# Kernel tuning notes

Hardware: AMD Instinct MI355X
Metric: run time of the kernel (lower is better)

The kernel has to match this reference:

```python
import jax, jax.numpy as jnp
import numpy as np

EPS = 1e-5  # float32 path of the torch LayerNorm variants


def setup_inputs() -> dict:
    key = jax.random.key(0)
    ks = jax.random.split(key, 12)
    b, c, t, h, w = 2, 512, 16, 32, 32
    heads, dim_head = 8, 64
    inner = heads * dim_head            # 512
    cpb = c // 2                        # 256 (ContinuousPositionBias hidden dim)
    inner_ff = int(c * 4 * 2 / 3)       # 1365 (GEGLU FeedForward)
    s = 0.02
    return {
        "x": jax.random.normal(ks[0], (b, c, t, h, w), jnp.float32),
        "framerate": 4,
        "g_norm": jnp.ones((c,), jnp.float32),
        "Wq": jax.random.normal(ks[1], (c, inner), jnp.float32) * s,
        "Wkv": jax.random.normal(ks[2], (c, 2 * inner), jnp.float32) * s,
        "Wo": jax.random.normal(ks[3], (inner, c), jnp.float32) * s,
        "pos_emb": jax.random.normal(ks[4], (1, 30, c), jnp.float32),
        "fr_emb": jax.random.normal(ks[5], (1, 30, c), jnp.float32),
        "cpb_w1": jax.random.normal(ks[6], (1, cpb), jnp.float32) * s,
        "cpb_b1": jnp.zeros((cpb,), jnp.float32),
        "cpb_w2": jax.random.normal(ks[7], (cpb, cpb), jnp.float32) * s,
        "cpb_b2": jnp.zeros((cpb,), jnp.float32),
        "cpb_w3": jax.random.normal(ks[8], (cpb, 8), jnp.float32) * s,
        "cpb_b3": jnp.zeros((8,), jnp.float32),
        "Win": jax.random.normal(ks[9], (c, 2 * inner_ff), jnp.float32) * s,
        "chan_g": jnp.ones((inner_ff,), jnp.float32),
        "Wout": jax.random.normal(ks[10], (inner_ff, c), jnp.float32) * s,
    }


def _forward(x, framerate, g_norm, Wq, Wkv, Wo, pos_emb, fr_emb,
             cpb_w1, cpb_b1, cpb_w2, cpb_b2, cpb_w3, cpb_b3,
             Win, chan_g, Wout):
    b, c, t, hh, ww = x.shape
    heads = cpb_b3.shape[0]
    dim_head = Wq.shape[1] // heads
    scale = dim_head ** -0.5

    # ---- ContinuousPositionBias over time (num_dims=1, log_dist) ----
    pos = jnp.arange(t)
    rel = (pos[:, None] - pos[None, :])[..., None].astype(x.dtype)   # [t, t, 1]
    rel = jnp.sign(rel) * jnp.log(jnp.abs(rel) + 1.0)
    hb = jax.nn.silu(rel @ cpb_w1 + cpb_b1)
    hb = jax.nn.silu(hb @ cpb_w2 + cpb_b2)
    bias = jnp.transpose(hb @ cpb_w3 + cpb_b3, (2, 0, 1))            # [H, t, t]

    # ---- temporal attention: fold spatial dims into batch ----
    xt = jnp.transpose(x, (0, 3, 4, 2, 1)).reshape(b * hh * ww, t, c)  # [B, t, c]
    xe = xt + pos_emb[:, :t] + fr_emb[:, framerate - 1:framerate]
    # LayerNorm as written in the source: stats over dim=1 (the token axis)
    mean = jnp.mean(xe, axis=1, keepdims=True)
    var = jnp.var(xe, axis=1, keepdims=True)
    xn = (xe - mean) * jax.lax.rsqrt(jnp.maximum(var, EPS)) * g_norm

    q = (xn @ Wq).reshape(-1, t, heads, dim_head).transpose(0, 2, 1, 3)  # [B,H,t,d]
    k, v = jnp.split(xn @ Wkv, 2, axis=-1)
    k = k.reshape(-1, t, heads, dim_head).transpose(0, 2, 1, 3)
    v = v.reshape(-1, t, heads, dim_head).transpose(0, 2, 1, 3)

    sim = jnp.einsum('bhid,bhjd->bhij', q * scale, k) + bias[None]
    attn = jax.nn.softmax(sim, axis=-1)
    o = jnp.einsum('bhij,bhjd->bhid', attn, v)
    o = o.transpose(0, 2, 1, 3).reshape(-1, t, heads * dim_head) @ Wo
    xt = o + xt  # residual
    x = jnp.transpose(xt.reshape(b, hh, ww, t, c), (0, 4, 3, 1, 2))  # [b,c,t,h,w]

    # ---- GEGLU FeedForward (1x1x1 convs) with token shift over time ----
    y = jnp.einsum('bcthw,co->bothw', x, Win)
    y1, gate = jnp.split(y, 2, axis=1)
    y = y1 * jax.nn.gelu(gate, approximate=False)
    half = (y.shape[1] + 1) // 2  # torch.chunk: first chunk gets ceil
    ya, yb = y[:, :half], y[:, half:]
    yb = jnp.pad(yb, ((0, 0), (0, 0), (1, 0), (0, 0), (0, 0)))[:, :, :-1]
    y = jnp.concatenate([ya, yb], axis=1)
    m = jnp.mean(y, axis=1, keepdims=True)
    vv = jnp.var(y, axis=1, keepdims=True)
    y = (y - m) * jax.lax.rsqrt(jnp.maximum(vv, EPS)) * chan_g[None, :, None, None, None]
    y = jnp.einsum('bcthw,co->bothw', y, Wout)
    return y + x


def reference(x, framerate, g_norm, Wq, Wkv, Wo, pos_emb, fr_emb,
              cpb_w1, cpb_b1, cpb_w2, cpb_b2, cpb_w3, cpb_b3,
              Win, chan_g, Wout):
    return _forward(x, framerate, g_norm, Wq, Wkv, Wo, pos_emb, fr_emb,
                    cpb_w1, cpb_b1, cpb_w2, cpb_b2, cpb_w3, cpb_b3,
                    Win, chan_g, Wout)
```

## Files before the change

kernel.cpp:

```cpp
#include <hip/hip_runtime.h>

using u16 = unsigned short;
using f32x4 = __attribute__((ext_vector_type(4))) float;
using short8 = __attribute__((ext_vector_type(8))) short;

__device__ __forceinline__ float bf2f(u16 u) {
    union { unsigned int i; float f; } v; v.i = ((unsigned int)u) << 16; return v.f;
}
__device__ __forceinline__ u16 f2bf(float f) {
    union { float f; unsigned int i; } v; v.f = f;
    unsigned int u = v.i;
    u += 0x7fffu + ((u >> 16) & 1u);
    return (u16)(u >> 16);
}
__device__ __forceinline__ void gload16(const u16* g, u16* l) {
    __builtin_amdgcn_global_load_lds((const __attribute__((address_space(1))) void*)g,
                                     (__attribute__((address_space(3))) void*)l, 16, 0, 0);
}

__global__ __launch_bounds__(256) void prep_weights(
    const float* __restrict__ Wq, const float* __restrict__ Wkv,
    const float* __restrict__ Wo, const float* __restrict__ Win,
    const float* __restrict__ Wout, const float* __restrict__ cg,
    u16* __restrict__ wqkvt, u16* __restrict__ wot,
    u16* __restrict__ winp, u16* __restrict__ woutt)
{
    int i = blockIdx.x * 256 + threadIdx.x;
    if (i < 1536 * 512) {
        int n = i >> 9, c = i & 511;
        float v = (n < 512) ? Wq[c * 512 + n] : Wkv[c * 1024 + (n - 512)];
        wqkvt[i] = f2bf(v); return;
    }
    i -= 1536 * 512;
    if (i < 512 * 512) {
        int cc = i >> 9, k = i & 511;
        wot[i] = f2bf(Wo[k * 512 + cc]); return;
    }
    i -= 512 * 512;
    if (i < 2816 * 512) {
        int n = i >> 9, c = i & 511;
        int jj = ((n >> 5) << 4) + (n & 15);
        int gate = (n >> 4) & 1;
        float v = (jj < 1365) ? Win[c * 2730 + jj + gate * 1365] : 0.f;
        winp[i] = f2bf(v); return;
    }
    i -= 2816 * 512;
    if (i < 512 * 1408) {
        int cc = i / 1408, j = i % 1408;
        float v = (j < 1365) ? Wout[j * 512 + cc] * cg[j] : 0.f;
        woutt[i] = f2bf(v); return;
    }
}

__global__ __launch_bounds__(256) void ssum_kernel(
    const float* __restrict__ Wout, const float* __restrict__ cg, float* __restrict__ ssum)
{
    int c = blockIdx.x * 256 + threadIdx.x;
    if (c >= 512) return;
    float s = 0.f;
    for (int j = 0; j < 1365; ++j) s += Wout[j * 512 + c] * cg[j];
    ssum[c] = s;
}

__global__ __launch_bounds__(256) void bias_kernel(
    const float* __restrict__ w1, const float* __restrict__ b1,
    const float* __restrict__ w2, const float* __restrict__ b2,
    const float* __restrict__ w3, const float* __restrict__ b3,
    float* __restrict__ bias)
{
    __shared__ float h1[256], h2[256];
    int rc = blockIdx.x;
    int ti = rc >> 4, tj = rc & 15;
    int j = threadIdx.x;
    float r = (float)(ti - tj);
    float rl = (r > 0.f) ? logf(r + 1.f) : ((r < 0.f) ? -logf(1.f - r) : 0.f);
    float a = rl * w1[j] + b1[j];
    h1[j] = a / (1.f + __expf(-a));
    __syncthreads();
    float acc = b2[j];
    for (int k = 0; k < 256; ++k) acc += h1[k] * w2[k * 256 + j];
    h2[j] = acc / (1.f + __expf(-acc));
    __syncthreads();
    if (j < 8) {
        float ab = b3[j];
        for (int k = 0; k < 256; ++k) ab += h2[k] * w3[k * 8 + j];
        bias[j * 256 + ti * 16 + tj] = ab;
    }
}

__global__ __launch_bounds__(256) void k1_norm(
    const float* __restrict__ x, const int* __restrict__ frp,
    const float* __restrict__ g_norm, const float* __restrict__ pos_emb,
    const float* __restrict__ fr_emb,
    u16* __restrict__ xn, u16* __restrict__ xt)
{
    __shared__ u16 tile[256 * 34];
    const int bid = blockIdx.x;
    const int b = bid >> 10, rem = bid & 1023;
    const int hw0 = (rem >> 4) << 4;
    const int c0 = (rem & 15) << 5;
    const int tid = threadIdx.x;
    const int hwl = tid & 15, cl = tid >> 4;
    const int fr = frp[0] - 1;
    float v[2][16], mean2[2], ri2[2], gg2[2], fv2[2];
    for (int cp = 0; cp < 2; ++cp) {
        const int c = c0 + cl + (cp << 4);
        const float* xp = x + (size_t)(b * 512 + c) * 16384 + hw0 + hwl;
        const float fv = fr_emb[fr * 512 + c];
        float s1 = 0.f, s2 = 0.f;
#pragma unroll
        for (int t = 0; t < 16; ++t) {
            float xv = xp[t * 1024];
            v[cp][t] = xv;
            float xe = xv + pos_emb[t * 512 + c] + fv;
            s1 += xe; s2 += xe * xe;
        }
        float m = s1 * 0.0625f;
        float var = s2 * 0.0625f - m * m;
        mean2[cp] = m; ri2[cp] = rsqrtf(fmaxf(var, 1e-5f));
        gg2[cp] = g_norm[c]; fv2[cp] = fv;
    }
    for (int cp = 0; cp < 2; ++cp) {
        const int c = c0 + cl + (cp << 4);
#pragma unroll
        for (int t = 0; t < 16; ++t) {
            float xe = v[cp][t] + pos_emb[t * 512 + c] + fv2[cp];
            tile[((t << 4) + hwl) * 34 + cl + (cp << 4)] = f2bf((xe - mean2[cp]) * ri2[cp] * gg2[cp]);
        }
    }
    __syncthreads();
    for (int it = 0; it < 32; ++it) {
        int rowl = (tid >> 5) + (it << 3);
        int col = tid & 31;
        size_t p = (size_t)b * 16384 + (size_t)(rowl >> 4) * 1024 + hw0 + (rowl & 15);
        xn[p * 512 + c0 + col] = tile[rowl * 34 + col];
    }
    __syncthreads();
    for (int cp = 0; cp < 2; ++cp)
#pragma unroll
        for (int t = 0; t < 16; ++t)
            tile[((t << 4) + hwl) * 34 + cl + (cp << 4)] = f2bf(v[cp][t]);
    __syncthreads();
    for (int it = 0; it < 32; ++it) {
        int rowl = (tid >> 5) + (it << 3);
        int col = tid & 31;
        size_t p = (size_t)b * 16384 + (size_t)(rowl >> 4) * 1024 + hw0 + (rowl & 15);
        xt[p * 512 + c0 + col] = tile[rowl * 34 + col];
    }
}

template<int EPI>
__global__ __launch_bounds__(256, 2) void gemm_bt(
    const u16* __restrict__ A, const u16* __restrict__ B, int K, int Nb,
    u16* __restrict__ outb, float* __restrict__ outf,
    const u16* __restrict__ addb,
    const float* __restrict__ marr, const float* __restrict__ rinv,
    const float* __restrict__ ssum, int ldOut)
{
    __shared__ u16 lds[2 * 128 * 64];
    u16* lA = lds;
    u16* lB = lds + 128 * 64;
    const int tid = threadIdx.x, lane = tid & 63, w = tid >> 6;
    const int wr = w >> 1, wc = w & 1;
    const int cpx = gridDim.x >> 3;
    const int wgid = (blockIdx.x & 7) * cpx + (blockIdx.x >> 3);
    const int p0 = (wgid / Nb) * 128, n0 = (wgid % Nb) * 128;
    f32x4 acc[4][4] = {};
    for (int kt = 0; kt < K; kt += 64) {
        for (int i = 0; i < 4; ++i) {
            int rb = w * 4 + i;
            int r = rb * 8 + (lane >> 3);
            int cg = (lane & 7) ^ (r & 7);
            gload16(A + (size_t)(p0 + r) * K + (kt + cg * 8), lA + rb * 512);
            gload16(B + (size_t)(n0 + r) * K + (kt + cg * 8), lB + rb * 512);
        }
        __syncthreads();
#pragma unroll
        for (int kk = 0; kk < 2; ++kk) {
            short8 av[4], bv[4];
#pragma unroll
            for (int m = 0; m < 4; ++m) {
                int r = wr * 64 + m * 16 + (lane & 15);
                int cc = ((kk << 2) + (lane >> 4)) ^ (r & 7);
                av[m] = *(const short8*)(lA + r * 64 + cc * 8);
            }
#pragma unroll
            for (int n = 0; n < 4; ++n) {
                int r = wc * 64 + n * 16 + (lane & 15);
                int cc = ((kk << 2) + (lane >> 4)) ^ (r & 7);
                bv[n] = *(const short8*)(lB + r * 64 + cc * 8);
            }
#pragma unroll
            for (int m = 0; m < 4; ++m)
#pragma unroll
                for (int n = 0; n < 4; ++n)
                    acc[m][n] = __builtin_amdgcn_mfma_f32_16x16x32_bf16(av[m], bv[n], acc[m][n], 0, 0, 0);
        }
        __syncthreads();
    }

    if constexpr (EPI == 0 || EPI == 1) {
#pragma unroll
        for (int m = 0; m < 4; ++m)
#pragma unroll
            for (int n = 0; n < 4; ++n) {
                int row = p0 + wr * 64 + m * 16 + ((lane >> 4) << 2);
                int col = n0 + wc * 64 + n * 16 + (lane & 15);
#pragma unroll
                for (int r = 0; r < 4; ++r) {
                    float vv = acc[m][n][r];
                    if constexpr (EPI == 1) vv += bf2f(addb[(size_t)(row + r) * ldOut + col]);
                    outb[(size_t)(row + r) * ldOut + col] = f2bf(vv);
                }
            }
    } else if constexpr (EPI == 2) {
#pragma unroll
        for (int m = 0; m < 4; ++m)
#pragma unroll
            for (int np = 0; np < 2; ++np) {
                int nv = np << 1;
                int colBase = n0 + wc * 64 + nv * 16 + (lane & 15);
                int jj = ((colBase >> 5) << 4) + (colBase & 15);
                int rowb = p0 + wr * 64 + m * 16 + ((lane >> 4) << 2);
                int t = (rowb >> 10) & 15;
#pragma unroll
                for (int r = 0; r < 4; ++r) {
                    int p = rowb + r;
                    float vv = acc[m][nv][r], gv = acc[m][nv + 1][r];
                    float glu = vv * 0.5f * gv * (1.f + erff(gv * 0.70710678f));
                    if (jj >= 1365) {
                        outb[(size_t)p * 1408 + jj] = 0;
                    } else if (jj >= 683) {
                        if (t < 15) outb[(size_t)(p + 1024) * 1408 + jj] = f2bf(glu);
                        if (t == 0) outb[(size_t)p * 1408 + jj] = 0;
                    } else {
                        outb[(size_t)p * 1408 + jj] = f2bf(glu);
                    }
                }
            }
    } else {
        float* ldsT = (float*)lds;
        const int bb = p0 >> 14, tt = (p0 >> 10) & 15, hwb = p0 & 1023;
        float* outp = outf + (size_t)bb * 8388608 + (size_t)tt * 1024 + hwb;
        for (int cg4 = 0; cg4 < 4; ++cg4) {
            __syncthreads();
            if (wc == (cg4 >> 1)) {
#pragma unroll
                for (int m = 0; m < 4; ++m)
#pragma unroll
                    for (int nn = 0; nn < 2; ++nn) {
                        int n = ((cg4 & 1) << 1) + nn;
                        int cl2 = (nn << 4) + (lane & 15);
                        int col = n0 + wc * 64 + n * 16 + (lane & 15);
                        int rl = wr * 64 + m * 16 + ((lane >> 4) << 2);
                        float ssv = ssum[col];
#pragma unroll
                        for (int r = 0; r < 4; ++r) {
                            int p = p0 + rl + r;
                            float vv = rinv[p] * (acc[m][n][r] - marr[p] * ssv)
                                     + bf2f(addb[(size_t)p * 512 + col]);
                            ldsT[cl2 * 132 + rl + r] = vv;
                        }
                    }
            }
            __syncthreads();
#pragma unroll
            for (int e = 0; e < 16; ++e) {
                int li = e * 256 + tid;
                int cl2 = li >> 7, hwl = li & 127;
                outp[(size_t)(n0 + cg4 * 32 + cl2) * 16384 + hwl] = ldsT[cl2 * 132 + hwl];
            }
        }
    }
}

__global__ __launch_bounds__(256, 1) void attn_kernel(
    const u16* __restrict__ qkv, const float* __restrict__ bias, u16* __restrict__ o)
{
    __shared__ u16 qkvt[3 * 256 * 64];
    __shared__ float pl[256 * 17];
    __shared__ float bl[256];
    const int tid = threadIdx.x, lane = tid & 63, w = tid >> 6;
    const int pc = blockIdx.x, h = blockIdx.y;
    const int b = pc >> 6, hw0 = (pc & 63) << 4;
    bl[tid] = bias[h * 256 + tid];
    for (int i = 0; i < 24; ++i) {
        int idx = w * 24 + i;
        int s = idx >> 5, rb = idx & 31;
        int r = (rb << 3) + (lane >> 3);
        int cg = (lane & 7) ^ (r & 7);
        size_t grow = (size_t)b * 16384 + (size_t)(r >> 4) * 1024 + hw0 + (r & 15);
        gload16(qkv + grow * 1536 + s * 512 + h * 64 + cg * 8, qkvt + s * 16384 + rb * 512);
    }
    __syncthreads();
    {
        const int ti = tid >> 4, pix = tid & 15;
        float qv[64];
        const u16* qr = qkvt + tid * 64;
#pragma unroll
        for (int cc = 0; cc < 8; ++cc) {
            short8 qq = *(const short8*)(qr + ((cc ^ (tid & 7)) << 3));
#pragma unroll
            for (int j = 0; j < 8; ++j) qv[cc * 8 + j] = bf2f((u16)qq[j]);
        }
        float sc[16];
        for (int tj = 0; tj < 16; ++tj) {
            int rk = (tj << 4) + pix;
            const u16* kr = qkvt + 16384 + rk * 64;
            float a = 0.f;
#pragma unroll
            for (int cc = 0; cc < 8; ++cc) {
                short8 kk = *(const short8*)(kr + ((cc ^ (rk & 7)) << 3));
#pragma unroll
                for (int j = 0; j < 8; ++j) a += qv[cc * 8 + j] * bf2f((u16)kk[j]);
            }
            sc[tj] = a * 0.125f + bl[(ti << 4) + tj];
        }
        float mx = sc[0];
#pragma unroll
        for (int j = 1; j < 16; ++j) mx = fmaxf(mx, sc[j]);
        float sum = 0.f;
#pragma unroll
        for (int j = 0; j < 16; ++j) { sc[j] = __expf(sc[j] - mx); sum += sc[j]; }
        float inv = 1.f / sum;
#pragma unroll
        for (int j = 0; j < 16; ++j) pl[((pix << 4) + ti) * 17 + j] = sc[j] * inv;
    }
    __syncthreads();
    {
        const int pix = tid >> 4, dg = tid & 15;
        for (int ti = 0; ti < 16; ++ti) {
            float a0 = 0, a1 = 0, a2 = 0, a3 = 0;
            const float* pr = pl + ((pix << 4) + ti) * 17;
#pragma unroll
            for (int tj = 0; tj < 16; ++tj) {
                float pv = pr[tj];
                int rv = (tj << 4) + pix;
                const u16* vr = qkvt + 32768 + rv * 64 + (((dg >> 1) ^ (rv & 7)) << 3) + ((dg & 1) << 2);
                a0 += pv * bf2f(vr[0]); a1 += pv * bf2f(vr[1]);
                a2 += pv * bf2f(vr[2]); a3 += pv * bf2f(vr[3]);
            }
            size_t p = (size_t)b * 16384 + (size_t)ti * 1024 + hw0 + pix;
            uint2 pk;
            pk.x = (unsigned int)f2bf(a0) | ((unsigned int)f2bf(a1) << 16);
            pk.y = (unsigned int)f2bf(a2) | ((unsigned int)f2bf(a3) << 16);
            *(uint2*)(o + p * 512 + h * 64 + (dg << 2)) = pk;
        }
    }
}

__global__ __launch_bounds__(256) void stats_kernel(
    const u16* __restrict__ yg, float* __restrict__ marr, float* __restrict__ rinvv)
{
    const int lane = threadIdx.x & 63, w = threadIdx.x >> 6;
    const int gw = blockIdx.x * 4 + w;
    for (int rr = 0; rr < 16; ++rr) {
        int row = gw * 16 + rr;
        const u16* rp = yg + (size_t)row * 1408;
        float s = 0.f, q = 0.f;
        for (int it = 0; it < 3; ++it) {
            int qi = it * 64 + lane;
            if (qi < 176) {
                uint4 d = *(const uint4*)(rp + qi * 8);
#pragma unroll
                for (int e = 0; e < 4; ++e) {
                    unsigned int dd = (&d.x)[e];
                    float f0 = bf2f((u16)(dd & 0xffff)), f1 = bf2f((u16)(dd >> 16));
                    s += f0 + f1;
                    q += f0 * f0 + f1 * f1;
                }
            }
        }
        for (int off = 32; off; off >>= 1) { s += __shfl_xor(s, off); q += __shfl_xor(q, off); }
        if (lane == 0) {
            float m = s * (1.f / 1365.f);
            float var = q * (1.f / 1365.f) - m * m;
            marr[row] = m;
            rinvv[row] = rsqrtf(fmaxf(var, 1e-5f));
        }
    }
}

extern "C" void kernel_launch(void* const* d_in, const int* in_sizes, int n_in,
                              void* d_out, int out_size, void* d_ws, size_t ws_size,
                              hipStream_t stream)
{
    const float* x       = (const float*)d_in[0];
    const int*   frp     = (const int*)d_in[1];
    const float* g_norm  = (const float*)d_in[2];
    const float* Wq      = (const float*)d_in[3];
    const float* Wkv     = (const float*)d_in[4];
    const float* Wo      = (const float*)d_in[5];
    const float* pos_emb = (const float*)d_in[6];
    const float* fr_emb  = (const float*)d_in[7];
    const float* w1      = (const float*)d_in[8];
    const float* b1      = (const float*)d_in[9];
    const float* w2      = (const float*)d_in[10];
    const float* b2      = (const float*)d_in[11];
    const float* w3      = (const float*)d_in[12];
    const float* b3      = (const float*)d_in[13];
    const float* Win     = (const float*)d_in[14];
    const float* chan_g  = (const float*)d_in[15];
    const float* Wout    = (const float*)d_in[16];

    char* ws = (char*)d_ws;
    u16*   wqkvt = (u16*)(ws + 0);
    u16*   wot   = (u16*)(ws + 1572864);
    u16*   winp  = (u16*)(ws + 2097152);
    u16*   woutt = (u16*)(ws + 4980736);
    float* ssum  = (float*)(ws + 6422528);
    float* biasb = (float*)(ws + 6424576);
    float* marr  = (float*)(ws + 6432768);
    float* rinvv = (float*)(ws + 6563840);
    u16*   qkv   = (u16*)(ws + 8388608);
    u16*   xn    = (u16*)(ws + 109051904);
    u16*   xt    = (u16*)(ws + 142606336);
    u16*   x2    = (u16*)(ws + 176160768);
    u16*   o_att = xn;
    u16*   yg    = qkv;

    prep_weights<<<12544, 256, 0, stream>>>(Wq, Wkv, Wo, Win, Wout, chan_g, wqkvt, wot, winp, woutt);
    ssum_kernel<<<2, 256, 0, stream>>>(Wout, chan_g, ssum);
    bias_kernel<<<256, 256, 0, stream>>>(w1, b1, w2, b2, w3, b3, biasb);
    k1_norm<<<2048, 256, 0, stream>>>(x, frp, g_norm, pos_emb, fr_emb, xn, xt);
    gemm_bt<0><<<256 * 12, 256, 0, stream>>>(xn, wqkvt, 512, 12, qkv, nullptr, nullptr,
                                             nullptr, nullptr, nullptr, 1536);
    attn_kernel<<<dim3(128, 8), 256, 0, stream>>>(qkv, biasb, o_att);
    gemm_bt<1><<<256 * 4, 256, 0, stream>>>(o_att, wot, 512, 4, x2, nullptr, xt,
                                            nullptr, nullptr, nullptr, 512);
    gemm_bt<2><<<256 * 22, 256, 0, stream>>>(x2, winp, 512, 22, yg, nullptr, nullptr,
                                             nullptr, nullptr, nullptr, 1408);
    stats_kernel<<<512, 256, 0, stream>>>(yg, marr, rinvv);
    gemm_bt<3><<<256 * 4, 256, 0, stream>>>(yg, woutt, 1408, 4, nullptr, (float*)d_out, x2,
                                            marr, rinvv, ssum, 512);
}
```

Before: 463.4 us.

## Fuse channel-norm stats into final GEMM, retile attention, parallelize ssum

Drops the separate stats kernel: the final GEMM now sums values and squares of the A-tile rows while loading them from LDS (wc==0 waves only) and computes mean and rsqrt in its epilogue. The attention kernel is retiled to 8 pixels per block with half the LDS so two blocks fit per CU, and the work is split across all 256 threads in each phase. ssum is parallelized to one wave per column with a shuffle reduction. Risks: extra VALU work inside the GEMM inner loop for EPI 3, and load imbalance between waves.

```diff
diff --git a/kernel.cpp b/kernel.cpp
--- a/kernel.cpp
+++ b/kernel.cpp
@@ -52,14 +52,15 @@
     }
 }
 
-__global__ __launch_bounds__(256) void ssum_kernel(
+__global__ __launch_bounds__(64) void ssum_kernel(
     const float* __restrict__ Wout, const float* __restrict__ cg, float* __restrict__ ssum)
 {
-    int c = blockIdx.x * 256 + threadIdx.x;
-    if (c >= 512) return;
+    int c = blockIdx.x;
+    int lane = threadIdx.x;
     float s = 0.f;
-    for (int j = 0; j < 1365; ++j) s += Wout[j * 512 + c] * cg[j];
-    ssum[c] = s;
+    for (int j = lane; j < 1365; j += 64) s += Wout[j * 512 + c] * cg[j];
+    for (int off = 32; off; off >>= 1) s += __shfl_xor(s, off);
+    if (lane == 0) ssum[c] = s;
 }
 
 __global__ __launch_bounds__(256) void bias_kernel(
@@ -154,10 +155,10 @@
     const u16* __restrict__ A, const u16* __restrict__ B, int K, int Nb,
     u16* __restrict__ outb, float* __restrict__ outf,
     const u16* __restrict__ addb,
-    const float* __restrict__ marr, const float* __restrict__ rinv,
     const float* __restrict__ ssum, int ldOut)
 {
     __shared__ u16 lds[2 * 128 * 64];
+    __shared__ float smr[256];
     u16* lA = lds;
     u16* lB = lds + 128 * 64;
     const int tid = threadIdx.x, lane = tid & 63, w = tid >> 6;
@@ -166,6 +167,7 @@
     const int wgid = (blockIdx.x & 7) * cpx + (blockIdx.x >> 3);
     const int p0 = (wgid / Nb) * 128, n0 = (wgid % Nb) * 128;
     f32x4 acc[4][4] = {};
+    float sst[4] = {}, sq[4] = {};
     for (int kt = 0; kt < K; kt += 64) {
         for (int i = 0; i < 4; ++i) {
             int rb = w * 4 + i;
@@ -189,6 +191,17 @@
                 int r = wc * 64 + n * 16 + (lane & 15);
                 int cc = ((kk << 2) + (lane >> 4)) ^ (r & 7);
                 bv[n] = *(const short8*)(lB + r * 64 + cc * 8);
+            }
+            if constexpr (EPI == 3) {
+                if (wc == 0) {
+#pragma unroll
+                    for (int m = 0; m < 4; ++m)
+#pragma unroll
+                        for (int j = 0; j < 8; ++j) {
+                            float v = bf2f((u16)av[m][j]);
+                            sst[m] += v; sq[m] += v * v;
+                        }
+                }
             }
 #pragma unroll
             for (int m = 0; m < 4; ++m)
@@ -239,6 +252,25 @@
                 }
             }
     } else {
+        if (wc == 0) {
+#pragma unroll
+            for (int m = 0; m < 4; ++m) {
+                float s = sst[m], q = sq[m];
+                s += __shfl_xor(s, 16); q += __shfl_xor(q, 16);
+                s += __shfl_xor(s, 32); q += __shfl_xor(q, 32);
+                if ((lane >> 4) == 0) {
+                    int row = wr * 64 + m * 16 + (lane & 15);
+                    smr[row] = s; smr[128 + row] = q;
+                }
+            }
+        }
+        __syncthreads();
+        if (tid < 128) {
+            float mm = smr[tid] * (1.f / 1365.f);
+            float var = smr[128 + tid] * (1.f / 1365.f) - mm * mm;
+            smr[tid] = mm;
+            smr[128 + tid] = rsqrtf(fmaxf(var, 1e-5f));
+        }
         float* ldsT = (float*)lds;
         const int bb = p0 >> 14, tt = (p0 >> 10) & 15, hwb = p0 & 1023;
         float* outp = outf + (size_t)bb * 8388608 + (size_t)tt * 1024 + hwb;
@@ -257,7 +289,7 @@
 #pragma unroll
                         for (int r = 0; r < 4; ++r) {
                             int p = p0 + rl + r;
-                            float vv = rinv[p] * (acc[m][n][r] - marr[p] * ssv)
+                            float vv = smr[128 + rl + r] * (acc[m][n][r] - smr[rl + r] * ssv)
                                      + bf2f(addb[(size_t)p * 512 + col]);
                             ldsT[cl2 * 132 + rl + r] = vv;
                         }
@@ -274,39 +306,41 @@
     }
 }
 
-__global__ __launch_bounds__(256, 1) void attn_kernel(
+__global__ __launch_bounds__(256, 2) void attn_kernel(
     const u16* __restrict__ qkv, const float* __restrict__ bias, u16* __restrict__ o)
 {
-    __shared__ u16 qkvt[3 * 256 * 64];
-    __shared__ float pl[256 * 17];
+    __shared__ u16 qkvt[3 * 128 * 64];
+    __shared__ float pl[128 * 17];
     __shared__ float bl[256];
     const int tid = threadIdx.x, lane = tid & 63, w = tid >> 6;
     const int pc = blockIdx.x, h = blockIdx.y;
-    const int b = pc >> 6, hw0 = (pc & 63) << 4;
+    const int b = pc >> 7, hw0 = (pc & 127) << 3;
     bl[tid] = bias[h * 256 + tid];
-    for (int i = 0; i < 24; ++i) {
-        int idx = w * 24 + i;
-        int s = idx >> 5, rb = idx & 31;
+    for (int i = 0; i < 12; ++i) {
+        int idx = w * 12 + i;
+        int s = idx >> 4, rb = idx & 15;
         int r = (rb << 3) + (lane >> 3);
         int cg = (lane & 7) ^ (r & 7);
-        size_t grow = (size_t)b * 16384 + (size_t)(r >> 4) * 1024 + hw0 + (r & 15);
-        gload16(qkv + grow * 1536 + s * 512 + h * 64 + cg * 8, qkvt + s * 16384 + rb * 512);
+        size_t grow = (size_t)b * 16384 + (size_t)(r >> 3) * 1024 + hw0 + (r & 7);
+        gload16(qkv + grow * 1536 + s * 512 + h * 64 + cg * 8, qkvt + s * 8192 + rb * 512);
     }
     __syncthreads();
     {
-        const int ti = tid >> 4, pix = tid & 15;
+        const int qrow = tid & 127, hh = tid >> 7;
+        const int pix = qrow & 7, ti = qrow >> 3;
         float qv[64];
-        const u16* qr = qkvt + tid * 64;
+        const u16* qr = qkvt + qrow * 64;
 #pragma unroll
         for (int cc = 0; cc < 8; ++cc) {
-            short8 qq = *(const short8*)(qr + ((cc ^ (tid & 7)) << 3));
+            short8 qq = *(const short8*)(qr + ((cc ^ (qrow & 7)) << 3));
 #pragma unroll
             for (int j = 0; j < 8; ++j) qv[cc * 8 + j] = bf2f((u16)qq[j]);
         }
-        float sc[16];
-        for (int tj = 0; tj < 16; ++tj) {
-            int rk = (tj << 4) + pix;
-            const u16* kr = qkvt + 16384 + rk * 64;
+#pragma unroll
+        for (int tj8 = 0; tj8 < 8; ++tj8) {
+            int tj = (hh << 3) + tj8;
+            int rk = (tj << 3) + pix;
+            const u16* kr = qkvt + 8192 + rk * 64;
             float a = 0.f;
 #pragma unroll
             for (int cc = 0; cc < 8; ++cc) {
@@ -314,8 +348,14 @@
 #pragma unroll
                 for (int j = 0; j < 8; ++j) a += qv[cc * 8 + j] * bf2f((u16)kk[j]);
             }
-            sc[tj] = a * 0.125f + bl[(ti << 4) + tj];
-        }
+            pl[qrow * 17 + tj] = a * 0.125f + bl[(ti << 4) + tj];
+        }
+    }
+    __syncthreads();
+    if (tid < 128) {
+        float sc[16];
+#pragma unroll
+        for (int j = 0; j < 16; ++j) sc[j] = pl[tid * 17 + j];
         float mx = sc[0];
 #pragma unroll
         for (int j = 1; j < 16; ++j) mx = fmaxf(mx, sc[j]);
@@ -324,59 +364,33 @@
         for (int j = 0; j < 16; ++j) { sc[j] = __expf(sc[j] - mx); sum += sc[j]; }
         float inv = 1.f / sum;
 #pragma unroll
-        for (int j = 0; j < 16; ++j) pl[((pix << 4) + ti) * 17 + j] = sc[j] * inv;
+        for (int j = 0; j < 16; ++j) pl[tid * 17 + j] = sc[j] * inv;
     }
     __syncthreads();
     {
-        const int pix = tid >> 4, dg = tid & 15;
+        const int pix = tid >> 5, dg = tid & 31;
+        float v0[16], v1[16];
+#pragma unroll
+        for (int tj = 0; tj < 16; ++tj) {
+            int rv = (tj << 3) + pix;
+            unsigned int d = *(const unsigned int*)(qkvt + 16384 + rv * 64 +
+                               (((dg >> 2) ^ (rv & 7)) << 3) + ((dg & 3) << 1));
+            v0[tj] = bf2f((u16)(d & 0xffff));
+            v1[tj] = bf2f((u16)(d >> 16));
+        }
+#pragma unroll
         for (int ti = 0; ti < 16; ++ti) {
-            float a0 = 0, a1 = 0, a2 = 0, a3 = 0;
-            const float* pr = pl + ((pix << 4) + ti) * 17;
+            float a0 = 0.f, a1 = 0.f;
+            const float* pr = pl + ((ti << 3) + pix) * 17;
 #pragma unroll
             for (int tj = 0; tj < 16; ++tj) {
                 float pv = pr[tj];
-                int rv = (tj << 4) + pix;
-                const u16* vr = qkvt + 32768 + rv * 64 + (((dg >> 1) ^ (rv & 7)) << 3) + ((dg & 1) << 2);
-                a0 += pv * bf2f(vr[0]); a1 += pv * bf2f(vr[1]);
-                a2 += pv * bf2f(vr[2]); a3 += pv * bf2f(vr[3]);
+                a0 += pv * v0[tj];
+                a1 += pv * v1[tj];
             }
             size_t p = (size_t)b * 16384 + (size_t)ti * 1024 + hw0 + pix;
-            uint2 pk;
-            pk.x = (unsigned int)f2bf(a0) | ((unsigned int)f2bf(a1) << 16);
-            pk.y = (unsigned int)f2bf(a2) | ((unsigned int)f2bf(a3) << 16);
-            *(uint2*)(o + p * 512 + h * 64 + (dg << 2)) = pk;
-        }
-    }
-}
-
-__global__ __launch_bounds__(256) void stats_kernel(
-    const u16* __restrict__ yg, float* __restrict__ marr, float* __restrict__ rinvv)
-{
-    const int lane = threadIdx.x & 63, w = threadIdx.x >> 6;
-    const int gw = blockIdx.x * 4 + w;
-    for (int rr = 0; rr < 16; ++rr) {
-        int row = gw * 16 + rr;
-        const u16* rp = yg + (size_t)row * 1408;
-        float s = 0.f, q = 0.f;
-        for (int it = 0; it < 3; ++it) {
-            int qi = it * 64 + lane;
-            if (qi < 176) {
-                uint4 d = *(const uint4*)(rp + qi * 8);
-#pragma unroll
-                for (int e = 0; e < 4; ++e) {
-                    unsigned int dd = (&d.x)[e];
-                    float f0 = bf2f((u16)(dd & 0xffff)), f1 = bf2f((u16)(dd >> 16));
-                    s += f0 + f1;
-                    q += f0 * f0 + f1 * f1;
-                }
-            }
-        }
-        for (int off = 32; off; off >>= 1) { s += __shfl_xor(s, off); q += __shfl_xor(q, off); }
-        if (lane == 0) {
-            float m = s * (1.f / 1365.f);
-            float var = q * (1.f / 1365.f) - m * m;
-            marr[row] = m;
-            rinvv[row] = rsqrtf(fmaxf(var, 1e-5f));
+            unsigned int pk = (unsigned int)f2bf(a0) | ((unsigned int)f2bf(a1) << 16);
+            *(unsigned int*)(o + p * 512 + h * 64 + (dg << 1)) = pk;
         }
     }
 }
@@ -410,8 +424,6 @@
     u16*   woutt = (u16*)(ws + 4980736);
     float* ssum  = (float*)(ws + 6422528);
     float* biasb = (float*)(ws + 6424576);
-    float* marr  = (float*)(ws + 6432768);
-    float* rinvv = (float*)(ws + 6563840);
     u16*   qkv   = (u16*)(ws + 8388608);
     u16*   xn    = (u16*)(ws + 109051904);
     u16*   xt    = (u16*)(ws + 142606336);
@@ -420,17 +432,16 @@
     u16*   yg    = qkv;
 
     prep_weights<<<12544, 256, 0, stream>>>(Wq, Wkv, Wo, Win, Wout, chan_g, wqkvt, wot, winp, woutt);
-    ssum_kernel<<<2, 256, 0, stream>>>(Wout, chan_g, ssum);
+    ssum_kernel<<<512, 64, 0, stream>>>(Wout, chan_g, ssum);
     bias_kernel<<<256, 256, 0, stream>>>(w1, b1, w2, b2, w3, b3, biasb);
     k1_norm<<<2048, 256, 0, stream>>>(x, frp, g_norm, pos_emb, fr_emb, xn, xt);
     gemm_bt<0><<<256 * 12, 256, 0, stream>>>(xn, wqkvt, 512, 12, qkv, nullptr, nullptr,
-                                             nullptr, nullptr, nullptr, 1536);
-    attn_kernel<<<dim3(128, 8), 256, 0, stream>>>(qkv, biasb, o_att);
+                                             nullptr, 1536);
+    attn_kernel<<<dim3(256, 8), 256, 0, stream>>>(qkv, biasb, o_att);
     gemm_bt<1><<<256 * 4, 256, 0, stream>>>(o_att, wot, 512, 4, x2, nullptr, xt,
-                                            nullptr, nullptr, nullptr, 512);
+                                            nullptr, 512);
     gemm_bt<2><<<256 * 22, 256, 0, stream>>>(x2, winp, 512, 22, yg, nullptr, nullptr,
-                                             nullptr, nullptr, nullptr, 1408);
-    stats_kernel<<<512, 256, 0, stream>>>(yg, marr, rinvv);
+                                             nullptr, 1408);
     gemm_bt<3><<<256 * 4, 256, 0, stream>>>(yg, woutt, 1408, 4, nullptr, (float*)d_out, x2,
-                                            marr, rinvv, ssum, 512);
-}
+                                            ssum, 512);
+}
```

After: 437.6 us. 5.6% less time.
